# Optimization experiments

Measured on AMD Instinct MI355X. Metric: run time of the kernel, lower is better.

## Reference

```python
import jax, jax.numpy as jnp
import numpy as np

B, S, D, UNITS = 4, 2048, 4096, 4096

def setup_inputs() -> dict:
    key = jax.random.key(0)
    k1, k2 = jax.random.split(key)
    x = jax.random.normal(k1, (B, S, D), dtype=jnp.float32)
    # int8 quantized kernel, values in [-127, 127]
    quantized_kernel = jax.random.randint(k2, (D, UNITS), -127, 128, dtype=jnp.int32).astype(jnp.int8)
    scale = jnp.float32(0.02)
    return {"x": x, "quantized_kernel": quantized_kernel, "scale": scale}

def reference(x, quantized_kernel, scale):
    # Dequantize int8 weights to fp32 and apply linear transform: y = x @ (W_int8 * scale)
    kernel_fp32 = quantized_kernel.astype(jnp.float32) * scale
    return jnp.einsum("bsd,du->bsu", x, kernel_fp32)
```

## Files before the change

kernel.cpp:

```cpp
#include <hip/hip_runtime.h>
#include <cstdint>

typedef unsigned short u16;
typedef __bf16 bf16x8 __attribute__((ext_vector_type(8)));
typedef float f32x4 __attribute__((ext_vector_type(4)));
typedef int   i32x4 __attribute__((ext_vector_type(4)));
typedef u16   u16x4 __attribute__((ext_vector_type(4)));

#define M_DIM 8192
#define N_DIM 4096
#define K_DIM 4096

#define GLOBAL_AS(p) ((const __attribute__((address_space(1))) void*)(p))
#define LDS_AS(p)    ((__attribute__((address_space(3))) void*)(p))

__device__ __forceinline__ u16 f2bf(float f) {
    union { float f; uint32_t u; } x; x.f = f;
    uint32_t u = x.u;
    uint32_t r = (u + 0x7fffu + ((u >> 16) & 1u)) >> 16;
    return (u16)r;
}

__global__ __launch_bounds__(256) void prepass_kernel(const float* __restrict__ X,
                                                      const int* __restrict__ W,
                                                      u16* __restrict__ Xb,
                                                      u16* __restrict__ Wt) {
    const int bid = blockIdx.x;
    const int t   = threadIdx.x;
    if (bid < 4096) {
        __shared__ int tile[64][65];
        const int n0 = (bid & 63) * 64;
        const int k0 = (bid >> 6) * 64;
#pragma unroll
        for (int i = 0; i < 4; i++) {
            int e = t + i * 256;
            int r = e >> 4;
            int c = (e & 15) * 4;
            i32x4 v = __builtin_nontemporal_load(
                (const i32x4*)(W + (size_t)(k0 + r) * N_DIM + n0 + c));
            tile[r][c] = v.x; tile[r][c + 1] = v.y; tile[r][c + 2] = v.z; tile[r][c + 3] = v.w;
        }
        __syncthreads();
        {
            int n = t >> 2, ks = (t & 3) * 16;
            __align__(16) u16 o[16];
#pragma unroll
            for (int i = 0; i < 16; i++)
                o[i] = f2bf((float)tile[ks + i][n]);
            u16* dst = Wt + (size_t)(n0 + n) * K_DIM + k0 + ks;
            *(uint4*)(dst)     = *(const uint4*)&o[0];
            *(uint4*)(dst + 8) = *(const uint4*)&o[8];
        }
    } else {
        const size_t base = (size_t)(bid - 4096) * 4096;
        const f32x4*   x4 = (const f32x4*)X;
        u16x4*         o4 = (u16x4*)Xb;
#pragma unroll
        for (int it = 0; it < 8; it++) {
            size_t ia = base + (size_t)it * 512 + t;
            size_t ib = ia + 256;
            f32x4 a = __builtin_nontemporal_load(x4 + ia);
            f32x4 b = __builtin_nontemporal_load(x4 + ib);
            u16x4 oa, ob;
            oa.x = f2bf(a.x); oa.y = f2bf(a.y); oa.z = f2bf(a.z); oa.w = f2bf(a.w);
            ob.x = f2bf(b.x); ob.y = f2bf(b.y); ob.z = f2bf(b.z); ob.w = f2bf(b.w);
            o4[ia] = oa;
            o4[ib] = ob;
        }
    }
}


#define BK 64
#define NT (K_DIM / BK)
static_assert(NT >= 4 && (NT & 1) == 0, "tile count must be even and >= 4");

#define BARRIER() do { asm volatile("" ::: "memory"); \
                       __builtin_amdgcn_s_barrier();  \
                       asm volatile("" ::: "memory"); } while (0)
#define WAIT_LGKM() asm volatile("s_waitcnt lgkmcnt(0)" ::: "memory")
#define VMCNT(n)    asm volatile("s_waitcnt vmcnt(" #n ")" ::: "memory")

#define READ_A(dst, mhv)                                                          \
    _Pragma("unroll") for (int i = 0; i < 4; i++) {                               \
        const char* p_ = As_ + ((mhv) * 128 + wrow * 64 + i * 16 + fr) * 128;     \
        _Pragma("unroll") for (int kk = 0; kk < 2; kk++)                          \
            dst[i][kk] = *(const bf16x8*)(p_ + ((kk * 64 + fk2) ^ sw));           \
    }

#define READ_B(dst, nhv)                                                          \
    _Pragma("unroll") for (int j = 0; j < 2; j++) {                               \
        const char* p_ = Bs_ + ((nhv) * 128 + wcol * 32 + j * 16 + fr) * 128;     \
        _Pragma("unroll") for (int kk = 0; kk < 2; kk++)                          \
            dst[j][kk] = *(const bf16x8*)(p_ + ((kk * 64 + fk2) ^ sw));           \
    }

#define MFMA_Q(MH, NH, aarr, barr)                                                \
    do {                                                                          \
        __builtin_amdgcn_s_setprio(1);                                            \
        _Pragma("unroll") for (int kk = 0; kk < 2; kk++)                          \
            _Pragma("unroll") for (int i = 0; i < 4; i++)                         \
                _Pragma("unroll") for (int j = 0; j < 2; j++)                     \
                    acc[MH][NH][i][j] = __builtin_amdgcn_mfma_f32_16x16x32_bf16(  \
                        aarr[i][kk], barr[j][kk], acc[MH][NH][i][j], 0, 0, 0);    \
        __builtin_amdgcn_s_setprio(0);                                            \
    } while (0)

#define STAGE_A(bufv, h, kt)                                                      \
    do {                                                                          \
        const u16* g_ = gA + (size_t)(h) * (128 * K_DIM) + (kt) * 64;             \
        char* l_ = (char*)lds + (bufv) * 32768 + (h) * 16384 + wv * 1024;         \
        __builtin_amdgcn_global_load_lds(GLOBAL_AS(g_ + aoff0), LDS_AS(l_), 16, 0, 0);        \
        __builtin_amdgcn_global_load_lds(GLOBAL_AS(g_ + aoff1), LDS_AS(l_ + 8192), 16, 0, 0); \
    } while (0)

#define STAGE_B(bufv, h, kt)                                                      \
    do {                                                                          \
        const u16* g_ = gB + (size_t)(h) * (128 * K_DIM) + (kt) * 64;             \
        char* l_ = (char*)lds + 65536 + (bufv) * 32768 + (h) * 16384 + wv * 1024; \
        __builtin_amdgcn_global_load_lds(GLOBAL_AS(g_ + aoff0), LDS_AS(l_), 16, 0, 0);        \
        __builtin_amdgcn_global_load_lds(GLOBAL_AS(g_ + aoff1), LDS_AS(l_ + 8192), 16, 0, 0); \
    } while (0)

#define TILE(bv, S1, S2, S3, S4, SYNC)                                            \
    {                                                                             \
        const char* As_ = (const char*)lds + (bv) * 32768;                        \
        const char* Bs_ = (const char*)lds + 65536 + (bv) * 32768;                \
        bf16x8 a0[4][2], a1[4][2], b0[2][2], b1[2][2];                            \
                                                                         \
        READ_A(a0, 0); READ_B(b0, 0);                                             \
        S1;                                                                       \
        BARRIER(); WAIT_LGKM();                                                   \
        MFMA_Q(0, 0, a0, b0);                                                     \
        BARRIER();                                                                \
                                                                         \
        READ_B(b1, 1);                                                            \
        S2;                                                                       \
        BARRIER(); WAIT_LGKM();                                                   \
        MFMA_Q(0, 1, a0, b1);                                                     \
        BARRIER();                                                                \
                                                                         \
        READ_A(a1, 1);                                                            \
        S3;                                                                       \
        BARRIER(); WAIT_LGKM();                                                   \
        MFMA_Q(1, 0, a1, b0);                                                     \
        BARRIER();                                                                \
                                                                         \
        S4;                                                                       \
        BARRIER();                                                                \
        MFMA_Q(1, 1, a1, b1);                                                     \
        SYNC;                                                                     \
        BARRIER();                                                                \
    }

__global__ __launch_bounds__(512, 2) void gemm_bf16_kernel(const u16* __restrict__ A,
                                                           const u16* __restrict__ Bt,
                                                           const float* __restrict__ scale_p,
                                                           float* __restrict__ C) {
    __shared__ __align__(16) u16 lds[65536];

    const int tid  = threadIdx.x;
    const int lane = tid & 63;
    const int wv   = tid >> 6;
    const int wrow = wv >> 2;
    const int wcol = wv & 3;

    const int bid = blockIdx.x;
    const int wg  = ((bid & 7) << 6) | (bid >> 3);
    const size_t m0 = (size_t)(wg >> 4) * 256;
    const size_t n0 = (size_t)(wg & 15) * 256;

    const int fr  = lane & 15;
    const int fk2 = (lane >> 4) * 16;
    const int sw  = (lane & 7) << 4;

    const int q0 = tid,       r0 = q0 >> 3, c0 = (q0 & 7) ^ (r0 & 7);
    const int q1 = tid + 512, r1 = q1 >> 3, c1 = (q1 & 7) ^ (r1 & 7);
    const size_t aoff0 = (size_t)r0 * K_DIM + c0 * 8;
    const size_t aoff1 = (size_t)r1 * K_DIM + c1 * 8;

    const u16* gA = A  + m0 * K_DIM;
    const u16* gB = Bt + n0 * K_DIM;

    f32x4 acc[2][2][4][2] = {};

    STAGE_A(0, 0, 0);
    STAGE_B(0, 0, 0);
    STAGE_B(0, 1, 0);
    STAGE_A(0, 1, 0);
    STAGE_A(1, 0, 1);
    STAGE_B(1, 0, 1);
    STAGE_B(1, 1, 1);
    VMCNT(6);
    BARRIER();

#pragma unroll 2
    for (int T = 0; T < NT - 2; ++T) {
        const int b  = T & 1;
        const int bo = b ^ 1;
        TILE(b,
             STAGE_A(bo, 1, T + 1),
             STAGE_A(b,  0, T + 2),
             STAGE_B(b,  0, T + 2),
             STAGE_B(b,  1, T + 2),
             VMCNT(6));
    }
    TILE(0, STAGE_A(1, 1, NT - 1), , , , VMCNT(0));
    TILE(1, , , , , );

    const float s = *scale_p;
    const int ec = lane & 15;
    const int er = (lane >> 4) * 4;
#pragma unroll
    for (int mh = 0; mh < 2; mh++)
#pragma unroll
        for (int nh = 0; nh < 2; nh++)
#pragma unroll
            for (int i = 0; i < 4; i++)
#pragma unroll
                for (int j = 0; j < 2; j++) {
                    float* cp = C + (m0 + mh * 128 + wrow * 64 + i * 16 + er) * N_DIM
                                  + (n0 + nh * 128 + wcol * 32 + j * 16 + ec);
#pragma unroll
                    for (int r = 0; r < 4; r++)
                        __builtin_nontemporal_store(acc[mh][nh][i][j][r] * s,
                                                    cp + (size_t)r * N_DIM);
                }
}

__global__ __launch_bounds__(256) void fb_gemm_kernel(const float* __restrict__ X,
                                                      const int* __restrict__ W,
                                                      const float* __restrict__ sp,
                                                      float* __restrict__ Y) {
    __shared__ float Xs[16][64];
    __shared__ float Ws[16][64];
    const int t = threadIdx.x;
    const int tx = t & 15, ty = t >> 4;
    const int m0 = blockIdx.y * 64, n0 = blockIdx.x * 64;
    float acc[4][4] = {};
    for (int k0 = 0; k0 < K_DIM; k0 += 16) {
#pragma unroll
        for (int i = 0; i < 4; i++) {
            int e = t + i * 256;
            int r = e >> 4, c = e & 15;
            Xs[c][r] = X[(size_t)(m0 + r) * K_DIM + k0 + c];
            int rw = e >> 6, cw = e & 63;
            Ws[rw][cw] = (float)W[(size_t)(k0 + rw) * N_DIM + n0 + cw];
        }
        __syncthreads();
#pragma unroll
        for (int kk = 0; kk < 16; kk++)
#pragma unroll
            for (int i = 0; i < 4; i++)
#pragma unroll
                for (int j = 0; j < 4; j++)
                    acc[i][j] += Xs[kk][ty * 4 + i] * Ws[kk][tx * 4 + j];
        __syncthreads();
    }
    const float s = *sp;
#pragma unroll
    for (int i = 0; i < 4; i++)
#pragma unroll
        for (int j = 0; j < 4; j++)
            Y[(size_t)(m0 + ty * 4 + i) * N_DIM + n0 + tx * 4 + j] = acc[i][j] * s;
}

extern "C" void kernel_launch(void* const* d_in, const int* in_sizes, int n_in,
                              void* d_out, int out_size, void* d_ws, size_t ws_size,
                              hipStream_t stream) {
    const float* X  = (const float*)d_in[0];
    const int*   W  = (const int*)d_in[1];
    const float* sp = (const float*)d_in[2];
    float* Y = (float*)d_out;

    const size_t xb = (size_t)M_DIM * K_DIM * sizeof(u16);
    const size_t wb = (size_t)N_DIM * K_DIM * sizeof(u16);

    if (ws_size >= xb + wb) {
        u16* Xb = (u16*)d_ws;
        u16* Wt = (u16*)((char*)d_ws + xb);
        prepass_kernel<<<6144, 256, 0, stream>>>(X, W, Xb, Wt);
        gemm_bf16_kernel<<<512, 512, 0, stream>>>(Xb, Wt, sp, Y);
    } else {
        fb_gemm_kernel<<<dim3(N_DIM / 64, M_DIM / 64), 256, 0, stream>>>(X, W, sp, Y);
    }
}
```

Before: 470.3 us.

## Restructure GEMM main loop to prefetch next tile fragments and cut barriers

Rewrites the K-loop schedule so each quarter-tile has a single barrier, and the A0/B0 fragments of the next LDS buffer are read into registers during the current tile's last MFMA quarters. The loop is unrolled by two with fixed buffer indices, and staging loads are reordered so each buffer is refilled whole. The aim is to hide LDS read latency behind MFMAs and drop about half of the workgroup barriers. In exchange the fragment registers stay live across tiles, which raises register pressure, and the tighter buffer reuse depends on correct vmcnt and barrier placement.

```diff
diff --git a/kernel.cpp b/kernel.cpp
--- a/kernel.cpp
+++ b/kernel.cpp
@@ -73,7 +73,7 @@
 
 #define BK 64
 #define NT (K_DIM / BK)
-static_assert(NT >= 4 && (NT & 1) == 0, "tile count must be even and >= 4");
+static_assert(NT >= 6 && (NT & 1) == 0, "tile count must be even and >= 6");
 
 #define BARRIER() do { asm volatile("" ::: "memory"); \
                        __builtin_amdgcn_s_barrier();  \
@@ -81,16 +81,16 @@
 #define WAIT_LGKM() asm volatile("s_waitcnt lgkmcnt(0)" ::: "memory")
 #define VMCNT(n)    asm volatile("s_waitcnt vmcnt(" #n ")" ::: "memory")
 
-#define READ_A(dst, mhv)                                                          \
+#define READ_A(dst, base, mhv)                                                    \
     _Pragma("unroll") for (int i = 0; i < 4; i++) {                               \
-        const char* p_ = As_ + ((mhv) * 128 + wrow * 64 + i * 16 + fr) * 128;     \
+        const char* p_ = (base) + ((mhv) * 128 + wrow * 64 + i * 16 + fr) * 128;  \
         _Pragma("unroll") for (int kk = 0; kk < 2; kk++)                          \
             dst[i][kk] = *(const bf16x8*)(p_ + ((kk * 64 + fk2) ^ sw));           \
     }
 
-#define READ_B(dst, nhv)                                                          \
+#define READ_B(dst, base, nhv)                                                    \
     _Pragma("unroll") for (int j = 0; j < 2; j++) {                               \
-        const char* p_ = Bs_ + ((nhv) * 128 + wcol * 32 + j * 16 + fr) * 128;     \
+        const char* p_ = (base) + ((nhv) * 128 + wcol * 32 + j * 16 + fr) * 128;  \
         _Pragma("unroll") for (int kk = 0; kk < 2; kk++)                          \
             dst[j][kk] = *(const bf16x8*)(p_ + ((kk * 64 + fk2) ^ sw));           \
     }
@@ -108,7 +108,7 @@
 
 #define STAGE_A(bufv, h, kt)                                                      \
     do {                                                                          \
-        const u16* g_ = gA + (size_t)(h) * (128 * K_DIM) + (kt) * 64;             \
+        const u16* g_ = gA + (size_t)(h) * (128 * K_DIM) + (size_t)(kt) * 64;     \
         char* l_ = (char*)lds + (bufv) * 32768 + (h) * 16384 + wv * 1024;         \
         __builtin_amdgcn_global_load_lds(GLOBAL_AS(g_ + aoff0), LDS_AS(l_), 16, 0, 0);        \
         __builtin_amdgcn_global_load_lds(GLOBAL_AS(g_ + aoff1), LDS_AS(l_ + 8192), 16, 0, 0); \
@@ -116,41 +116,38 @@
 
 #define STAGE_B(bufv, h, kt)                                                      \
     do {                                                                          \
-        const u16* g_ = gB + (size_t)(h) * (128 * K_DIM) + (kt) * 64;             \
+        const u16* g_ = gB + (size_t)(h) * (128 * K_DIM) + (size_t)(kt) * 64;     \
         char* l_ = (char*)lds + 65536 + (bufv) * 32768 + (h) * 16384 + wv * 1024; \
         __builtin_amdgcn_global_load_lds(GLOBAL_AS(g_ + aoff0), LDS_AS(l_), 16, 0, 0);        \
         __builtin_amdgcn_global_load_lds(GLOBAL_AS(g_ + aoff1), LDS_AS(l_ + 8192), 16, 0, 0); \
     } while (0)
 
-#define TILE(bv, S1, S2, S3, S4, SYNC)                                            \
+#define TILE(bv, S1, S2, S3, S4, VM2, PRE)                                        \
     {                                                                             \
         const char* As_ = (const char*)lds + (bv) * 32768;                        \
         const char* Bs_ = (const char*)lds + 65536 + (bv) * 32768;                \
-        bf16x8 a0[4][2], a1[4][2], b0[2][2], b1[2][2];                            \
-                                                                         \
-        READ_A(a0, 0); READ_B(b0, 0);                                             \
+        const char* An_ = (const char*)lds + ((bv) ^ 1) * 32768;                  \
+        const char* Bn_ = (const char*)lds + 65536 + ((bv) ^ 1) * 32768;          \
+                                                                         \
+        BARRIER(); WAIT_LGKM();                                                   \
+        READ_B(b1, Bs_, 1);                                                       \
         S1;                                                                       \
-        BARRIER(); WAIT_LGKM();                                                   \
         MFMA_Q(0, 0, a0, b0);                                                     \
-        BARRIER();                                                                \
-                                                                         \
-        READ_B(b1, 1);                                                            \
-        S2;                                                                       \
-        BARRIER(); WAIT_LGKM();                                                   \
+                                                                         \
+        BARRIER(); WAIT_LGKM();                                                   \
+        READ_A(a1, As_, 1);                                                       \
+        S2; VM2;                                                                  \
         MFMA_Q(0, 1, a0, b1);                                                     \
-        BARRIER();                                                                \
-                                                                         \
-        READ_A(a1, 1);                                                            \
+                                                                         \
+        BARRIER(); WAIT_LGKM();                                                   \
+        if (PRE) { READ_A(a0, An_, 0); }                                          \
         S3;                                                                       \
-        BARRIER(); WAIT_LGKM();                                                   \
         MFMA_Q(1, 0, a1, b0);                                                     \
-        BARRIER();                                                                \
-                                                                         \
+                                                                         \
+        BARRIER(); WAIT_LGKM();                                                   \
+        if (PRE) { READ_B(b0, Bn_, 0); }                                          \
         S4;                                                                       \
-        BARRIER();                                                                \
         MFMA_Q(1, 1, a1, b1);                                                     \
-        SYNC;                                                                     \
-        BARRIER();                                                                \
     }
 
 __global__ __launch_bounds__(512, 2) void gemm_bf16_kernel(const u16* __restrict__ A,
@@ -183,30 +180,32 @@
     const u16* gB = Bt + n0 * K_DIM;
 
     f32x4 acc[2][2][4][2] = {};
-
-    STAGE_A(0, 0, 0);
-    STAGE_B(0, 0, 0);
-    STAGE_B(0, 1, 0);
-    STAGE_A(0, 1, 0);
-    STAGE_A(1, 0, 1);
-    STAGE_B(1, 0, 1);
-    STAGE_B(1, 1, 1);
-    VMCNT(6);
+    bf16x8 a0[4][2], a1[4][2], b0[2][2], b1[2][2];
+
+    STAGE_A(0, 0, 0); STAGE_B(0, 0, 0); STAGE_B(0, 1, 0); STAGE_A(0, 1, 0);
+    STAGE_A(1, 0, 1); STAGE_B(1, 0, 1); STAGE_B(1, 1, 1); STAGE_A(1, 1, 1);
+    VMCNT(8);
     BARRIER();
-
-#pragma unroll 2
-    for (int T = 0; T < NT - 2; ++T) {
-        const int b  = T & 1;
-        const int bo = b ^ 1;
-        TILE(b,
-             STAGE_A(bo, 1, T + 1),
-             STAGE_A(b,  0, T + 2),
-             STAGE_B(b,  0, T + 2),
-             STAGE_B(b,  1, T + 2),
-             VMCNT(6));
-    }
-    TILE(0, STAGE_A(1, 1, NT - 1), , , , VMCNT(0));
-    TILE(1, , , , , );
+    {
+        const char* As_ = (const char*)lds;
+        const char* Bs_ = (const char*)lds + 65536;
+        READ_A(a0, As_, 0);
+        READ_B(b0, Bs_, 0);
+    }
+    WAIT_LGKM();
+
+    for (int T = 0; T < NT - 2; T += 2) {
+        TILE(0,
+             STAGE_A(0, 0, T + 2), STAGE_B(0, 0, T + 2),
+             STAGE_B(0, 1, T + 2), STAGE_A(0, 1, T + 2),
+             VMCNT(4), 1);
+        TILE(1,
+             STAGE_A(1, 0, T + 3), STAGE_B(1, 0, T + 3),
+             STAGE_B(1, 1, T + 3), STAGE_A(1, 1, T + 3),
+             VMCNT(4), 1);
+    }
+    TILE(0, (void)0, (void)0, (void)0, (void)0, VMCNT(0), 1);
+    TILE(1, (void)0, (void)0, (void)0, (void)0, (void)0, 0);
 
     const float s = *scale_p;
     const int ec = lane & 15;
```

Result: slower. 515.9 us (+9.7%).
